# Kernel optimization log

Measured on AMD Instinct MI355X. Metric: run time of the kernel, lower is better.

## Reference

```python
import jax, jax.numpy as jnp
import numpy as np

B = 1024      # batch
D_NUM = 100   # numeric features
N_CAT = 20    # categorical features
CARD = 100    # cardinality per categorical feature
D = 1024      # d_token
DH = 675      # int(d_token * 0.66)
NT = D_NUM + 1 + N_CAT  # 121 tokens (CLS + numeric + categorical)
E = 4         # num_experts
K = 2         # top_k
MID = 512     # ResidualHead mid dim = max(D//2, 16)
RH = 256      # router/alpha hidden = max(D//4, 16)


def _ln(x, g, b):
    m = x.mean(-1, keepdims=True)
    v = ((x - m) ** 2).mean(-1, keepdims=True)
    return (x - m) * jax.lax.rsqrt(v + 1e-5) * g + b


def setup_inputs() -> dict:
    key = jax.random.key(0)
    ks = jax.random.split(key, 20)

    def n(i, shape, s=0.02):
        return jax.random.normal(ks[i], shape, dtype=jnp.float32) * s

    return dict(
        x_num=jax.random.normal(ks[0], (B, D_NUM), dtype=jnp.float32),
        x_cat=jax.random.randint(ks[1], (B, N_CAT), 0, CARD),
        tok_w=n(2, (D_NUM + 1, D), 0.05),
        tok_b=n(3, (D_NUM + N_CAT, D), 0.05),
        cat_emb=n(4, (N_CAT * CARD, D), 0.05),
        ln_g=jnp.ones((D,), jnp.float32), ln_b=jnp.zeros((D,), jnp.float32),
        lin0_w=n(5, (D, 2 * DH)), lin0_b=jnp.zeros((2 * DH,), jnp.float32),
        sgu_ln_g=jnp.ones((DH,), jnp.float32), sgu_ln_b=jnp.zeros((DH,), jnp.float32),
        sgu_w=n(6, (NT, NT), 0.05), sgu_b=jnp.zeros((NT,), jnp.float32),
        lin1_w=n(7, (DH, D)), lin1_b=jnp.zeros((D,), jnp.float32),
        r_w1=n(8, (D, RH)), r_b1=jnp.zeros((RH,), jnp.float32),
        r_w2=n(9, (RH, E)), r_b2=jnp.zeros((E,), jnp.float32),
        a_w1=n(10, (D, RH)), a_b1=jnp.zeros((RH,), jnp.float32),
        a_w2=n(11, (RH, 1)), a_b2=jnp.full((1,), -4.0, jnp.float32),
        base_w=n(12, (D, 1)), base_b=jnp.zeros((1,), jnp.float32),
        gh_w1=n(13, (D, MID), 0.001), gh_b1=jnp.zeros((MID,), jnp.float32),
        gh_w2=n(14, (MID, 1), 0.001), gh_b2=jnp.zeros((1,), jnp.float32),
        ex_w1=n(15, (E, D, MID), 0.001), ex_b1=jnp.zeros((E, MID), jnp.float32),
        ex_w2=n(16, (E, MID), 0.001), ex_b2=jnp.zeros((E,), jnp.float32),
    )


def reference(x_num, x_cat, tok_w, tok_b, cat_emb, ln_g, ln_b, lin0_w, lin0_b,
              sgu_ln_g, sgu_ln_b, sgu_w, sgu_b, lin1_w, lin1_b,
              r_w1, r_b1, r_w2, r_b2, a_w1, a_b1, a_w2, a_b2,
              base_w, base_b, gh_w1, gh_b1, gh_w2, gh_b2,
              ex_w1, ex_b1, ex_w2, ex_b2):
    # ---- Tokenizer ----
    offsets = jnp.arange(N_CAT) * CARD
    xn = jnp.concatenate([jnp.ones((x_num.shape[0], 1), x_num.dtype), x_num], axis=1)  # [B, D_NUM+1]
    x = tok_w[None] * xn[:, :, None]                                  # [B, D_NUM+1, D]
    x = jnp.concatenate([x, cat_emb[x_cat + offsets[None]]], axis=1)  # [B, NT, D]
    bias_full = jnp.concatenate([jnp.zeros((1, D), tok_b.dtype), tok_b], axis=0)
    x = x + bias_full[None]
    # ---- gMLP layer (n_layers=1) ----
    xr = x
    h = _ln(x, ln_g, ln_b)
    h = jax.nn.gelu(h @ lin0_w + lin0_b, approximate=False)           # [B, NT, 2*DH]
    u, v = h[..., :DH], h[..., DH:]
    v = _ln(v, sgu_ln_g, sgu_ln_b)
    # SGU token-mixing: out[b,s,d] = sum_t v[b,t,d] * W[s,t] + bias[s]
    v = jnp.einsum('btd,st->bsd', v, sgu_w) + sgu_b[None, :, None]
    x = (u * v) @ lin1_w + lin1_b
    x = x + xr
    # ---- pooled hidden (CLS token) ----
    hidden = jax.nn.gelu(_ln(x[:, 0], ln_g, ln_b), approximate=False)  # [B, D]
    # ---- router + top-k sparsification ----
    logits = jax.nn.relu(hidden @ r_w1 + r_b1) @ r_w2 + r_b2           # [B, E]
    dense = jax.nn.softmax(logits, axis=-1)
    vals, idx = jax.lax.top_k(dense, K)
    sparse = jnp.zeros_like(dense).at[jnp.arange(dense.shape[0])[:, None], idx].set(vals)
    rw = sparse / jnp.clip(sparse.sum(-1, keepdims=True), 1e-8)
    # ---- local experts (small residual heads, vectorized over E) ----
    eh = jax.nn.relu(jnp.einsum('bd,edm->bem', hidden, ex_w1) + ex_b1[None])
    eo = jnp.einsum('bem,em->be', eh, ex_w2) + ex_b2[None]             # [B, E]
    local = (rw * eo).sum(-1, keepdims=True)                           # [B, 1]
    # ---- global residual, alpha gate, base head ----
    glob = jax.nn.relu(hidden @ gh_w1 + gh_b1) @ gh_w2 + gh_b2
    alpha = jax.nn.sigmoid(jax.nn.relu(hidden @ a_w1 + a_b1) @ a_w2 + a_b2)
    y_base = hidden @ base_w + base_b
    return y_base + alpha * (glob + local)                             # [B, 1]
```

## Files before the change

### kernel.cpp

```cpp
#include <hip/hip_runtime.h>
#include <math.h>

#define B_SZ 1024

typedef __attribute__((ext_vector_type(8))) short bf16x8;
typedef __attribute__((ext_vector_type(4))) float f32x4;
typedef __attribute__((ext_vector_type(4))) float floatx4;
typedef __attribute__((ext_vector_type(4))) unsigned short ushortx4;

#define GLOAD16(src, dst) __builtin_amdgcn_global_load_lds( \
    (const __attribute__((address_space(1))) void*)(src), \
    (__attribute__((address_space(3))) void*)(dst), 16, 0, 0)

__device__ __forceinline__ unsigned short f2bf(float f) {
  unsigned int u = __float_as_uint(f);
  u += 0x7fff + ((u >> 16) & 1);
  return (unsigned short)(u >> 16);
}
__device__ __forceinline__ float bf2f(unsigned short b) {
  return __uint_as_float(((unsigned int)b) << 16);
}
__device__ __forceinline__ float gelu_exact(float x) {
  return 0.5f * x * (1.0f + erff(x * 0.70710678118654752f));
}
__device__ __forceinline__ float gelu_fast(float x) {
  const float c0 = 2.3022586f;
  const float c1 = 0.10295465f;
  float z = x * __builtin_fmaf(x * x, c1, c0);
  float e = __builtin_amdgcn_exp2f(z);
  float r = __builtin_amdgcn_rcpf(e + 1.0f);
  return __builtin_fmaf(-x, r, x);
}
__device__ __forceinline__ float wred(float v) {
#pragma unroll
  for (int o = 32; o > 0; o >>= 1) v += __shfl_xor(v, o, 64);
  return v;
}

struct PrepArgs {
  const float* src[10];
  unsigned short* dst[10];
  int ldin[10]; int coff[10]; int Nsrc[10]; int Ksrc[10]; int Kp[10];
  int nbx[10]; int blk0[11];
};

__global__ __launch_bounds__(256)
void prep_all(PrepArgs J,
              const float* __restrict__ tok_w, const float* __restrict__ tok_b,
              const float* __restrict__ cat_emb,
              const float* __restrict__ ln_g, const float* __restrict__ ln_b,
              const float* __restrict__ r_b1, const float* __restrict__ a_b1,
              const float* __restrict__ gh_b1, const float* __restrict__ ex_b1,
              unsigned short* __restrict__ Amat,
              float* __restrict__ nstat, float* __restrict__ cstat,
              float* __restrict__ bcat)
{
  const int bid = blockIdx.x;
  const int tid = threadIdx.x;
  const int lane = tid & 63;
  const int NT = J.blk0[10];
  if (bid < NT) {
    __shared__ float tile[64][65];
    int j = 0;
    while (bid >= J.blk0[j + 1]) ++j;
    const int bx = bid - J.blk0[j];
    const int k0 = (bx % J.nbx[j]) * 64;
    const int n0 = (bx / J.nbx[j]) * 64;
    const float* in = J.src[j];
    unsigned short* out = J.dst[j];
    const int ldin = J.ldin[j], coff = J.coff[j], Nsrc = J.Nsrc[j], Ksrc = J.Ksrc[j], Kp = J.Kp[j];
    const int kx = tid & 63;
    const int ry = tid >> 6;
    for (int r = ry; r < 64; r += 4) {
      const int k = k0 + r;
      const int n = n0 + kx;
      tile[r][kx] = (k < Ksrc && n < Nsrc) ? in[(size_t)k * ldin + coff + n] : 0.f;
    }
    __syncthreads();
    for (int r = ry; r < 64; r += 4) {
      const int n = n0 + r;
      const int k = k0 + kx;
      out[(size_t)n * Kp + k] = f2bf(tile[kx][r]);
    }
  } else if (bid < NT + 576) {
    const int r = (bid - NT) * 4 + (tid >> 6);
    if (r >= 2304) return;
    unsigned short* out = Amat + (size_t)r * 1024;
    for (int k = lane * 4; k < 1024; k += 256) {
      floatx4 g = *(const floatx4*)(ln_g + k);
      floatx4 v;
      if (r <= 100) {
        floatx4 a = *(const floatx4*)(tok_w + (size_t)r * 1024 + k);
#pragma unroll
        for (int q = 0; q < 4; q++) v[q] = a[q] * g[q];
      } else if (r <= 200) {
        floatx4 a = *(const floatx4*)(tok_b + (size_t)(r - 101) * 1024 + k);
#pragma unroll
        for (int q = 0; q < 4; q++) v[q] = a[q] * g[q];
      } else if (r <= 2200) {
        const int j = r - 201;
        const int c = j / 100;
        floatx4 a = *(const floatx4*)(cat_emb + (size_t)j * 1024 + k);
        floatx4 bq = *(const floatx4*)(tok_b + (size_t)(100 + c) * 1024 + k);
#pragma unroll
        for (int q = 0; q < 4; q++) v[q] = (a[q] + bq[q]) * g[q];
      } else if (r == 2201) {
        v = g;
      } else if (r == 2202) {
        v = *(const floatx4*)(ln_b + k);
      } else {
        v[0] = 0.f; v[1] = 0.f; v[2] = 0.f; v[3] = 0.f;
      }
      ushortx4 o;
#pragma unroll
      for (int q = 0; q < 4; q++) o[q] = f2bf(v[q]);
      *(ushortx4*)(out + k) = o;
    }
  } else if (bid < NT + 576 + 526) {
    const int w = (bid - NT - 576) * 4 + (tid >> 6);
    if (w >= 2101) return;
    if (w <= 100) {
      const int t = w;
      const float* wr = tok_w + (size_t)t * 1024;
      const float* br = (t >= 1) ? (tok_b + (size_t)(t - 1) * 1024) : nullptr;
      float sw = 0, sww = 0, sb = 0, sbb = 0, swb = 0;
      for (int k = lane * 4; k < 1024; k += 256) {
        floatx4 a = *(const floatx4*)(wr + k);
#pragma unroll
        for (int q = 0; q < 4; q++) { sw += a[q]; sww += a[q] * a[q]; }
        if (br) {
          floatx4 bq = *(const floatx4*)(br + k);
#pragma unroll
          for (int q = 0; q < 4; q++) { sb += bq[q]; sbb += bq[q] * bq[q]; swb += a[q] * bq[q]; }
        }
      }
      sw = wred(sw); sww = wred(sww); sb = wred(sb); sbb = wred(sbb); swb = wred(swb);
      if (lane == 0) {
        float* ns = nstat + (size_t)t * 5;
        ns[0] = sw; ns[1] = sww; ns[2] = sb; ns[3] = sbb; ns[4] = swb;
      }
    } else {
      const int j = w - 101;
      const int c = j / 100;
      const float* ar = cat_emb + (size_t)j * 1024;
      const float* br = tok_b + (size_t)(100 + c) * 1024;
      float s1 = 0, s2 = 0;
      for (int k = lane * 4; k < 1024; k += 256) {
        floatx4 a = *(const floatx4*)(ar + k);
        floatx4 bq = *(const floatx4*)(br + k);
#pragma unroll
        for (int q = 0; q < 4; q++) { const float v = a[q] + bq[q]; s1 += v; s2 += v * v; }
      }
      s1 = wred(s1); s2 = wred(s2);
      if (lane == 0) { cstat[(size_t)j * 2] = s1; cstat[(size_t)j * 2 + 1] = s2; }
    }
  } else {
    const int n = (bid - NT - 1102) * 256 + tid;
    if (n >= 3072) return;
    float v;
    if (n < 256) v = r_b1[n];
    else if (n < 512) v = a_b1[n - 256];
    else if (n < 1024) v = gh_b1[n - 512];
    else v = ex_b1[n - 1024];
    bcat[n] = v;
  }
}

template<int EPI>
__device__ __forceinline__
void gemm_body(int bid, const unsigned short* __restrict__ A, long pitchA,
               const unsigned short* __restrict__ Bw, int K,
               const float* __restrict__ bias, int bias_off,
               const float* __restrict__ extra,
               int NB, int Nvalid, int ldo,
               float* __restrict__ outf, unsigned short* __restrict__ outb)
{
  __shared__ unsigned short As[128 * 32];
  __shared__ unsigned short Bs[128 * 32];
  const int tid = threadIdx.x, lane = tid & 63, wv = tid >> 6;
  const int nb = bid % NB, mb = bid / NB;
  const int m0 = mb * 128, n0 = nb * 128;
  const int wr = (wv >> 1) << 6, wc = (wv & 1) << 6;
  const int fr = lane & 15, fq = lane >> 4;
  const int c0 = wv * 2;
  const int srow = lane >> 2;
  const int sk = (lane & 3) << 3;

  const unsigned short* a0 = A + (size_t)(m0 + c0 * 16 + srow) * pitchA + sk;
  const unsigned short* a1 = A + (size_t)(m0 + (c0 + 1) * 16 + srow) * pitchA + sk;
  const unsigned short* b0p = Bw + (size_t)(n0 + c0 * 16 + srow) * K + sk;
  const unsigned short* b1p = Bw + (size_t)(n0 + (c0 + 1) * 16 + srow) * K + sk;

  f32x4 acc[4][4] = {};
  for (int k0 = 0; k0 < K; k0 += 32) {
    __syncthreads();
    GLOAD16(a0 + k0, &As[c0 * 512]);
    GLOAD16(a1 + k0, &As[(c0 + 1) * 512]);
    GLOAD16(b0p + k0, &Bs[c0 * 512]);
    GLOAD16(b1p + k0, &Bs[(c0 + 1) * 512]);
    __syncthreads();
    bf16x8 af[4], bw_[4];
#pragma unroll
    for (int i = 0; i < 4; i++) {
      af[i]  = *(const bf16x8*)&As[(wr + i * 16 + fr) * 32 + fq * 8];
      bw_[i] = *(const bf16x8*)&Bs[(wc + i * 16 + fr) * 32 + fq * 8];
    }
#pragma unroll
    for (int i = 0; i < 4; i++)
#pragma unroll
      for (int j = 0; j < 4; j++)
        acc[i][j] = __builtin_amdgcn_mfma_f32_16x16x32_bf16(af[i], bw_[j], acc[i][j], 0, 0, 0);
  }

#pragma unroll
  for (int i = 0; i < 4; i++)
#pragma unroll
    for (int j = 0; j < 4; j++) {
      const int n = n0 + wc + j * 16 + fr;
      if (n >= ldo) continue;
      const bool valid = (n < Nvalid);
      const float bv = (EPI == 3) ? 0.f : (valid ? bias[bias_off + n] : 0.f);
      const float ev = (EPI == 0) ? extra[n] : 0.f;
#pragma unroll
      for (int q = 0; q < 4; q++) {
        const int m = m0 + wr + i * 16 + fq * 4 + q;
        const float a = acc[i][j][q];
        if (EPI == 0) {
          outf[(size_t)m * ldo + n] = a + bv + ev;
        } else if (EPI == 1) {
          outb[(size_t)m * ldo + n] = f2bf(fmaxf(a + bv, 0.f));
        } else {
          outf[(size_t)m * ldo + n] = a;
        }
      }
    }
}

template<int EPI>
__global__ __launch_bounds__(256)
void gemm_gl(const unsigned short* __restrict__ A, long pitchA,
             const unsigned short* __restrict__ Bw, int K,
             const float* __restrict__ bias, int bias_off,
             const float* __restrict__ extra,
             int NB, int Nvalid, int ldo,
             float* __restrict__ outf, unsigned short* __restrict__ outb)
{
  gemm_body<EPI>(blockIdx.x, A, pitchA, Bw, K, bias, bias_off, extra, NB, Nvalid, ldo, outf, outb);
}

__device__ __forceinline__
void u_const_body(int bid, const unsigned short* __restrict__ w0u, const float* __restrict__ nstat,
                  const float* __restrict__ tok_w, const float* __restrict__ ln_g,
                  const float* __restrict__ ln_b, const float* __restrict__ lin0_b,
                  float* __restrict__ ucon)
{
  __shared__ float xk[1024];
  const int tid = threadIdx.x, lane = tid & 63, wv = tid >> 6;
  const float m = nstat[0] * (1.f / 1024.f);
  const float ex2 = nstat[1] * (1.f / 1024.f);
  const float rs = rsqrtf(ex2 - m * m + 1e-5f);
  for (int k = tid; k < 1024; k += 256)
    xk[k] = bf2f(f2bf((tok_w[k] - m) * rs * ln_g[k] + ln_b[k]));
  __syncthreads();
  const int c = bid * 4 + wv;
  if (c >= 704) return;
  if (c >= 675) { if (lane == 0) ucon[c] = 0.f; return; }
  const unsigned short* wr = w0u + (size_t)c * 1024;
  float s = 0.f;
  for (int k = lane; k < 1024; k += 64) s += bf2f(wr[k]) * xk[k];
  s = wred(s);
  if (lane == 0) ucon[c] = gelu_exact(s + lin0_b[c]);
}

__global__ __launch_bounds__(256)
void tab_and_u(const unsigned short* __restrict__ Amat, const unsigned short* __restrict__ w0v,
               float* __restrict__ TAB,
               const unsigned short* __restrict__ w0u, const float* __restrict__ nstat,
               const float* __restrict__ tok_w, const float* __restrict__ ln_g,
               const float* __restrict__ ln_b, const float* __restrict__ lin0_b,
               float* __restrict__ ucon)
{
  if (blockIdx.x < 108)
    gemm_body<3>(blockIdx.x, Amat, 1024, w0v, 1024, nullptr, 0, nullptr, 6, 768, 768, TAB, nullptr);
  else
    u_const_body(blockIdx.x - 108, w0u, nstat, tok_w, ln_g, ln_b, lin0_b, ucon);
}

__global__ __launch_bounds__(256)
void cat_rows(const float* __restrict__ TAB, const float* __restrict__ nstat,
              const float* __restrict__ cstat, const float* __restrict__ lin0_b,
              const float* __restrict__ sgu_w,
              float* __restrict__ catval, float* __restrict__ catsc,
              float* __restrict__ wss_g)
{
  const int r = blockIdx.x * 4 + (threadIdx.x >> 6);
  const int lane = threadIdx.x & 63;
  if (r == 2001) {
    float s = (lane < 121) ? sgu_w[lane] : 0.f;
    if (lane + 64 < 121) s += sgu_w[lane + 64];
    s = wred(s);
    if (lane == 0) wss_g[0] = s;
    return;
  }
  if (r > 2001) return;
  float m, ex2;
  const float* T1;
  if (r < 2000) {
    m = cstat[(size_t)r * 2] * (1.f / 1024.f);
    ex2 = cstat[(size_t)r * 2 + 1] * (1.f / 1024.f);
    T1 = TAB + (size_t)(201 + r) * 768;
  } else {
    m = nstat[0] * (1.f / 1024.f);
    ex2 = nstat[1] * (1.f / 1024.f);
    T1 = TAB;
  }
  const float rs = rsqrtf(ex2 - m * m + 1e-5f);
  const float ga = -m * rs;
  const float* R = TAB + (size_t)2201 * 768;
  const float* C = TAB + (size_t)2202 * 768;
  const int dl = lane << 2;
  float s = 0.f, ss = 0.f;
  float* outp = catval + (size_t)r * 768;
#pragma unroll
  for (int ch = 0; ch < 3; ch++) {
    const int d = ch * 256 + dl;
    floatx4 t1 = *(const floatx4*)(T1 + d);
    floatx4 rr = *(const floatx4*)(R + d);
    floatx4 cc = *(const floatx4*)(C + d);
    floatx4 o;
#pragma unroll
    for (int q = 0; q < 4; q++) {
      const int dd = d + q;
      const float c2 = (dd < 675) ? (cc[q] + lin0_b[675 + dd]) : 0.f;
      const float pre = __builtin_fmaf(rs, t1[q], __builtin_fmaf(ga, rr[q], c2));
      const float g = (dd < 675) ? gelu_fast(pre) : 0.f;
      o[q] = g; s += g; ss = __builtin_fmaf(g, g, ss);
    }
    *(floatx4*)(outp + d) = o;
  }
  s = wred(s); ss = wred(ss);
  const float mu = s * (1.f / 675.f);
  const float rho = rsqrtf(ss * (1.f / 675.f) - mu * mu + 1e-5f);
  if (lane == 0) { catsc[(size_t)r * 2] = mu; catsc[(size_t)r * 2 + 1] = rho; }
}

__global__ __launch_bounds__(512, 4)
void fused_v4(const float* __restrict__ TAB, const float* __restrict__ nstat,
              const float* __restrict__ catsc, const float* __restrict__ catval,
              const float* __restrict__ x_num, const int* __restrict__ x_cat,
              const float* __restrict__ sgu_ln_g, const float* __restrict__ sgu_ln_b,
              const float* __restrict__ sgu_w, const float* __restrict__ sgu_b,
              const float* __restrict__ lin0_b, const float* __restrict__ ucon,
              const float* __restrict__ wss_g,
              unsigned short* __restrict__ uv)
{
  const int b = blockIdx.x;
  const int tid = threadIdx.x, lane = tid & 63, wv = tid >> 6;
  __shared__ float Rls[768], Cls[768];
  __shared__ float alf[100], bet[100], gam[100], swt[100];
  __shared__ float wrc[21], catkb[21];
  __shared__ int catrowS[21];
  __shared__ float accw[8][768];
  __shared__ float kbw[8];

  for (int d = tid; d < 768; d += 512) {
    Rls[d] = (d < 675) ? TAB[(size_t)2201 * 768 + d] : 0.f;
    Cls[d] = (d < 675) ? (TAB[(size_t)2202 * 768 + d] + lin0_b[675 + d]) : 0.f;
  }
  if (tid < 100) {
    const int tt = tid;
    const float sc = x_num[b * 100 + tt];
    const float* ns = nstat + (size_t)(tt + 1) * 5;
    const float m = (sc * ns[0] + ns[2]) * (1.f / 1024.f);
    const float ex2 = (sc * sc * ns[1] + 2.f * sc * ns[4] + ns[3]) * (1.f / 1024.f);
    const float rs = rsqrtf(ex2 - m * m + 1e-5f);
    alf[tt] = rs * sc; bet[tt] = rs; gam[tt] = -m * rs;
    swt[tt] = sgu_w[tt + 1];
  } else if (tid < 121) {
    const int ii = tid - 100;
    int row; float sw;
    if (ii < 20) { row = x_cat[b * 20 + ii] + 100 * ii; sw = sgu_w[101 + ii]; }
    else { row = 2000; sw = sgu_w[0]; }
    const float mu = catsc[(size_t)row * 2], rho = catsc[(size_t)row * 2 + 1];
    const float wr = sw * rho;
    wrc[ii] = wr; catkb[ii] = wr * mu; catrowS[ii] = row;
  }
  __syncthreads();

  float acc[12] = {};
  float kb = 0.f;
  const int dl = lane << 2;

  for (int i = 0; i < 7; i++) {
    const int tA = wv + 16 * i;
    if (tA >= 100) break;
    const int tB = tA + 8;
    const bool hB = (tB < 100);
    const int tBs = hB ? tB : tA;
    const float aA = alf[tA], eA = bet[tA], gA = gam[tA];
    const float aB = alf[tBs], eB = bet[tBs], gB = gam[tBs];
    const float* T1A = TAB + (size_t)(tA + 1) * 768;
    const float* T2A = TAB + (size_t)(101 + tA) * 768;
    const float* T1B = TAB + (size_t)(tBs + 1) * 768;
    const float* T2B = TAB + (size_t)(101 + tBs) * 768;
    float vA[12], vB[12];
    float sA = 0.f, qA = 0.f, sB = 0.f, qB = 0.f;
#pragma unroll
    for (int ch = 0; ch < 3; ch++) {
      const int d = ch * 256 + dl;
      floatx4 t1a = *(const floatx4*)(T1A + d);
      floatx4 t2a = *(const floatx4*)(T2A + d);
      floatx4 t1b = *(const floatx4*)(T1B + d);
      floatx4 t2b = *(const floatx4*)(T2B + d);
      floatx4 rr = *(const floatx4*)(&Rls[d]);
      floatx4 cc = *(const floatx4*)(&Cls[d]);
#pragma unroll
      for (int q = 0; q < 4; q++) {
        const float g0 = gelu_fast(__builtin_fmaf(aA, t1a[q], __builtin_fmaf(eA, t2a[q], __builtin_fmaf(gA, rr[q], cc[q]))));
        vA[ch * 4 + q] = g0; sA += g0; qA = __builtin_fmaf(g0, g0, qA);
        const float g1 = gelu_fast(__builtin_fmaf(aB, t1b[q], __builtin_fmaf(eB, t2b[q], __builtin_fmaf(gB, rr[q], cc[q]))));
        vB[ch * 4 + q] = g1; sB += g1; qB = __builtin_fmaf(g1, g1, qB);
      }
    }
    sA = wred(sA); qA = wred(qA); sB = wred(sB); qB = wred(qB);
    const float swA = swt[tA];
    const float swB = hB ? swt[tBs] : 0.f;
    const float muA = sA * (1.f / 675.f);
    const float wA = swA * rsqrtf(qA * (1.f / 675.f) - muA * muA + 1e-5f);
    const float muB = sB * (1.f / 675.f);
    const float wB = swB * rsqrtf(qB * (1.f / 675.f) - muB * muB + 1e-5f);
#pragma unroll
    for (int q = 0; q < 12; q++)
      acc[q] = __builtin_fmaf(wA, vA[q], __builtin_fmaf(wB, vB[q], acc[q]));
    kb = __builtin_fmaf(wA, muA, __builtin_fmaf(wB, muB, kb));
  }

  for (int i = 0; i < 3; i++) {
    const int ii = wv + 8 * i;
    if (ii >= 21) break;
    const float wr = wrc[ii];
    const float* cv = catval + (size_t)catrowS[ii] * 768;
#pragma unroll
    for (int ch = 0; ch < 3; ch++) {
      floatx4 v = *(const floatx4*)(cv + ch * 256 + dl);
#pragma unroll
      for (int q = 0; q < 4; q++) acc[ch * 4 + q] = __builtin_fmaf(wr, v[q], acc[ch * 4 + q]);
    }
  }
  if (lane == 0) kbw[wv] = kb;

#pragma unroll
  for (int ch = 0; ch < 3; ch++)
    *(floatx4*)&accw[wv][ch * 256 + dl] = *(const floatx4*)&acc[ch * 4];
  __syncthreads();

  float kbs = 0.f;
#pragma unroll
  for (int w = 0; w < 8; w++) kbs += kbw[w];
#pragma unroll
  for (int i = 0; i < 21; i++) kbs += catkb[i];
  const float sb0 = sgu_b[0];
  const float wss = wss_g[0];
  for (int d = tid; d < 704; d += 512) {
    unsigned short o = 0;
    if (d < 675) {
      float a = 0.f;
#pragma unroll
      for (int w = 0; w < 8; w++) a += accw[w][d];
      const float v0 = sgu_ln_g[d] * (a - kbs) + sgu_ln_b[d] * wss + sb0;
      o = f2bf(ucon[d] * v0);
    }
    uv[(size_t)b * 704 + d] = o;
  }
}

__global__ __launch_bounds__(256)
void ln_gelu_hidden(const float* __restrict__ xfin,
                    const float* __restrict__ ln_g, const float* __restrict__ ln_b,
                    const float* __restrict__ base_w,
                    unsigned short* __restrict__ hid_bf, float* __restrict__ base_y)
{
  const int w = (blockIdx.x * 256 + threadIdx.x) >> 6;
  const int lane = threadIdx.x & 63;
  if (w >= B_SZ) return;
  const float* row = xfin + (size_t)w * 1024;
  float s = 0.f, ss = 0.f;
  for (int k = lane; k < 1024; k += 64) { float v = row[k]; s += v; ss += v * v; }
  s = wred(s); ss = wred(ss);
  const float m = s * (1.f / 1024.f);
  const float var = ss * (1.f / 1024.f) - m * m;
  const float rs = rsqrtf(var + 1e-5f);
  float bacc = 0.f;
  for (int k = lane; k < 1024; k += 64) {
    float v = gelu_fast((row[k] - m) * rs * ln_g[k] + ln_b[k]);
    hid_bf[(size_t)w * 1024 + k] = f2bf(v);
    bacc = __builtin_fmaf(v, base_w[k], bacc);
  }
  bacc = wred(bacc);
  if (lane == 0) base_y[w] = bacc;
}

__global__ __launch_bounds__(256)
void final_head(const unsigned short* __restrict__ H1, const float* __restrict__ base_y,
                const float* __restrict__ r_w2, const float* __restrict__ r_b2,
                const float* __restrict__ a_w2, const float* __restrict__ a_b2,
                const float* __restrict__ gh_w2, const float* __restrict__ gh_b2,
                const float* __restrict__ ex_w2, const float* __restrict__ ex_b2,
                const float* __restrict__ base_b,
                float* __restrict__ out)
{
  const int b = blockIdx.x;
  const int tid = threadIdx.x;
  const unsigned short* h1 = H1 + (size_t)b * 3072;
  float p[10];
#pragma unroll
  for (int i = 0; i < 10; i++) p[i] = 0.f;
  {
    const int m = tid;
    const float hr = bf2f(h1[m]);
    p[0] = hr * r_w2[m * 4 + 0];
    p[1] = hr * r_w2[m * 4 + 1];
    p[2] = hr * r_w2[m * 4 + 2];
    p[3] = hr * r_w2[m * 4 + 3];
    const float ha = bf2f(h1[256 + m]);
    p[4] = ha * a_w2[m];
  }
  for (int m = tid; m < 512; m += 256) {
    p[5] += bf2f(h1[512 + m]) * gh_w2[m];
#pragma unroll
    for (int e = 0; e < 4; e++)
      p[6 + e] += bf2f(h1[1024 + e * 512 + m]) * ex_w2[e * 512 + m];
  }

  __shared__ float red[10][4];
  const int lane = tid & 63, wv = tid >> 6;
#pragma unroll
  for (int i = 0; i < 10; i++) {
    const float v = wred(p[i]);
    if (lane == 0) red[i][wv] = v;
  }
  __syncthreads();
  if (tid == 0) {
    float s[10];
#pragma unroll
    for (int i = 0; i < 10; i++) s[i] = red[i][0] + red[i][1] + red[i][2] + red[i][3];
    float lg[4];
#pragma unroll
    for (int e = 0; e < 4; e++) lg[e] = s[e] + r_b2[e];
    const float mx = fmaxf(fmaxf(lg[0], lg[1]), fmaxf(lg[2], lg[3]));
    float den[4]; float dsum = 0.f;
#pragma unroll
    for (int e = 0; e < 4; e++) { den[e] = expf(lg[e] - mx); dsum += den[e]; }
#pragma unroll
    for (int e = 0; e < 4; e++) den[e] /= dsum;
    int i1 = 0;
    for (int e = 1; e < 4; e++) if (den[e] > den[i1]) i1 = e;
    int i2 = -1;
    for (int e = 0; e < 4; e++) { if (e == i1) continue; if (i2 < 0 || den[e] > den[i2]) i2 = e; }
    float eo[4];
#pragma unroll
    for (int e = 0; e < 4; e++) eo[e] = s[6 + e] + ex_b2[e];
    const float v1 = den[i1], v2 = den[i2];
    const float ssum = fmaxf(v1 + v2, 1e-8f);
    const float local = (v1 * eo[i1] + v2 * eo[i2]) / ssum;
    const float glob = s[5] + gh_b2[0];
    const float alpha = 1.0f / (1.0f + expf(-(s[4] + a_b2[0])));
    out[b] = base_y[b] + base_b[0] + alpha * (glob + local);
  }
}

extern "C" void kernel_launch(void* const* d_in, const int* in_sizes, int n_in,
                              void* d_out, int out_size, void* d_ws, size_t ws_size,
                              hipStream_t stream)
{
  const float* x_num  = (const float*)d_in[0];
  const int*   x_cat  = (const int*)d_in[1];
  const float* tok_w  = (const float*)d_in[2];
  const float* tok_b  = (const float*)d_in[3];
  const float* cat_emb= (const float*)d_in[4];
  const float* ln_g   = (const float*)d_in[5];
  const float* ln_b   = (const float*)d_in[6];
  const float* lin0_w = (const float*)d_in[7];
  const float* lin0_b = (const float*)d_in[8];
  const float* sgu_ln_g = (const float*)d_in[9];
  const float* sgu_ln_b = (const float*)d_in[10];
  const float* sgu_w  = (const float*)d_in[11];
  const float* sgu_b  = (const float*)d_in[12];
  const float* lin1_w = (const float*)d_in[13];
  const float* lin1_b = (const float*)d_in[14];
  const float* r_w1   = (const float*)d_in[15];
  const float* r_b1   = (const float*)d_in[16];
  const float* r_w2   = (const float*)d_in[17];
  const float* r_b2   = (const float*)d_in[18];
  const float* a_w1   = (const float*)d_in[19];
  const float* a_b1   = (const float*)d_in[20];
  const float* a_w2   = (const float*)d_in[21];
  const float* a_b2   = (const float*)d_in[22];
  const float* base_w = (const float*)d_in[23];
  const float* base_b = (const float*)d_in[24];
  const float* gh_w1  = (const float*)d_in[25];
  const float* gh_b1  = (const float*)d_in[26];
  const float* gh_w2  = (const float*)d_in[27];
  const float* gh_b2  = (const float*)d_in[28];
  const float* ex_w1  = (const float*)d_in[29];
  const float* ex_b1  = (const float*)d_in[30];
  const float* ex_w2  = (const float*)d_in[31];
  const float* ex_b2  = (const float*)d_in[32];
  (void)in_sizes; (void)n_in; (void)out_size; (void)ws_size;

  char* ws = (char*)d_ws;
  size_t off = 0;
  auto alloc = [&](size_t bytes) { void* p = ws + off; off += (bytes + 255) & ~(size_t)255; return p; };

  unsigned short* w0v  = (unsigned short*)alloc((size_t)768 * 1024 * 2);
  unsigned short* w0u  = (unsigned short*)alloc((size_t)768 * 1024 * 2);
  unsigned short* w1t  = (unsigned short*)alloc((size_t)1024 * 704 * 2);
  unsigned short* wcat = (unsigned short*)alloc((size_t)3072 * 1024 * 2);
  float* bcat          = (float*)alloc((size_t)3072 * 4);
  unsigned short* Amat = (unsigned short*)alloc((size_t)2304 * 1024 * 2);
  float* TAB           = (float*)alloc((size_t)2304 * 768 * 4);
  float* nstat         = (float*)alloc((size_t)101 * 5 * 4);
  float* cstat         = (float*)alloc((size_t)2000 * 2 * 4);
  float* catval        = (float*)alloc((size_t)2001 * 768 * 4);
  float* catsc         = (float*)alloc((size_t)2001 * 2 * 4);
  float* ucon          = (float*)alloc((size_t)704 * 4);
  float* wss_g         = (float*)alloc((size_t)4);
  unsigned short* uv   = (unsigned short*)alloc((size_t)B_SZ * 704 * 2);
  float* xfin          = (float*)alloc((size_t)B_SZ * 1024 * 4);
  float* base_y        = (float*)alloc((size_t)B_SZ * 4);
  unsigned short* hidb = (unsigned short*)alloc((size_t)B_SZ * 1024 * 2);
  unsigned short* H1   = (unsigned short*)alloc((size_t)B_SZ * 3072 * 2);

  const dim3 blk(256);

  PrepArgs J;
  auto setJ = [&](int i, const float* s, unsigned short* d, int ldin, int coff,
                  int Nsrc, int Ksrc, int Kp, int nbx, int nby) {
    J.src[i] = s; J.dst[i] = d; J.ldin[i] = ldin; J.coff[i] = coff;
    J.Nsrc[i] = Nsrc; J.Ksrc[i] = Ksrc; J.Kp[i] = Kp; J.nbx[i] = nbx;
    J.blk0[i + 1] = J.blk0[i] + nbx * nby;
  };
  J.blk0[0] = 0;
  setJ(0, lin0_w, w0v, 1350, 675, 675, 1024, 1024, 16, 12);
  setJ(1, lin0_w, w0u, 1350, 0,   675, 1024, 1024, 16, 12);
  setJ(2, lin1_w, w1t, 1024, 0,  1024,  675,  704, 11, 16);
  setJ(3, r_w1,  wcat,                          256, 0, 256, 1024, 1024, 16, 4);
  setJ(4, a_w1,  wcat + (size_t)256 * 1024,     256, 0, 256, 1024, 1024, 16, 4);
  setJ(5, gh_w1, wcat + (size_t)512 * 1024,     512, 0, 512, 1024, 1024, 16, 8);
  for (int e = 0; e < 4; e++)
    setJ(6 + e, ex_w1 + (size_t)e * 1024 * 512,
         wcat + (size_t)(1024 + e * 512) * 1024, 512, 0, 512, 1024, 1024, 16, 8);

  const int nprep = J.blk0[10] + 576 + 526 + 12;
  prep_all<<<nprep, blk, 0, stream>>>(J, tok_w, tok_b, cat_emb, ln_g, ln_b,
      r_b1, a_b1, gh_b1, ex_b1, Amat, nstat, cstat, bcat);

  tab_and_u<<<284, blk, 0, stream>>>(Amat, w0v, TAB, w0u, nstat, tok_w, ln_g, ln_b, lin0_b, ucon);

  cat_rows<<<501, blk, 0, stream>>>(TAB, nstat, cstat, lin0_b, sgu_w, catval, catsc, wss_g);

  fused_v4<<<B_SZ, dim3(512), 0, stream>>>(TAB, nstat, catsc, catval, x_num, x_cat,
      sgu_ln_g, sgu_ln_b, sgu_w, sgu_b, lin0_b, ucon, wss_g, uv);

  gemm_gl<0><<<8 * 8, blk, 0, stream>>>(uv, 704, w1t, 704,
      lin1_b, 0, tok_w, 8, 1024, 1024, xfin, nullptr);
  ln_gelu_hidden<<<B_SZ / 4, blk, 0, stream>>>(xfin, ln_g, ln_b, base_w, hidb, base_y);
  gemm_gl<1><<<8 * 24, blk, 0, stream>>>(hidb, 1024, wcat, 1024,
      bcat, 0, nullptr, 24, 3072, 3072, nullptr, H1);

  final_head<<<B_SZ, blk, 0, stream>>>(H1, base_y, r_w2, r_b2, a_w2, a_b2, gh_w2, gh_b2,
                                       ex_w2, ex_b2, base_b, (float*)d_out);
}
```

Baseline: 157.5 us.

## Shrink GEMM tiles to 64x64 and halve fused token-mixing block size

After: 165.6 us. +5.1%, slower.

```diff
diff --git a/kernel.cpp b/kernel.cpp
--- a/kernel.cpp
+++ b/kernel.cpp
@@ -168,58 +168,50 @@
 
 template<int EPI>
 __device__ __forceinline__
-void gemm_body(int bid, const unsigned short* __restrict__ A, long pitchA,
-               const unsigned short* __restrict__ Bw, int K,
-               const float* __restrict__ bias, int bias_off,
-               const float* __restrict__ extra,
-               int NB, int Nvalid, int ldo,
-               float* __restrict__ outf, unsigned short* __restrict__ outb)
-{
-  __shared__ unsigned short As[128 * 32];
-  __shared__ unsigned short Bs[128 * 32];
+void gemm64_body(int bid, const unsigned short* __restrict__ A, long pitchA,
+                 const unsigned short* __restrict__ Bw, int K,
+                 const float* __restrict__ bias, const float* __restrict__ extra,
+                 int NB, int Nvalid, int ldo,
+                 float* __restrict__ outf, unsigned short* __restrict__ outb)
+{
+  __shared__ unsigned short As[64 * 32];
+  __shared__ unsigned short Bs[64 * 32];
   const int tid = threadIdx.x, lane = tid & 63, wv = tid >> 6;
   const int nb = bid % NB, mb = bid / NB;
-  const int m0 = mb * 128, n0 = nb * 128;
-  const int wr = (wv >> 1) << 6, wc = (wv & 1) << 6;
+  const int m0 = mb * 64, n0 = nb * 64;
+  const int wr = (wv >> 1) << 5, wc = (wv & 1) << 5;
   const int fr = lane & 15, fq = lane >> 4;
-  const int c0 = wv * 2;
-  const int srow = lane >> 2;
-  const int sk = (lane & 3) << 3;
-
-  const unsigned short* a0 = A + (size_t)(m0 + c0 * 16 + srow) * pitchA + sk;
-  const unsigned short* a1 = A + (size_t)(m0 + (c0 + 1) * 16 + srow) * pitchA + sk;
-  const unsigned short* b0p = Bw + (size_t)(n0 + c0 * 16 + srow) * K + sk;
-  const unsigned short* b1p = Bw + (size_t)(n0 + (c0 + 1) * 16 + srow) * K + sk;
-
-  f32x4 acc[4][4] = {};
+
+  const unsigned short* srcA = A + (size_t)(m0 + (tid >> 2)) * pitchA + ((tid & 3) << 3);
+  const unsigned short* srcB = Bw + (size_t)(n0 + (tid >> 2)) * K + ((tid & 3) << 3);
+
+  f32x4 acc[2][2] = {};
   for (int k0 = 0; k0 < K; k0 += 32) {
     __syncthreads();
-    GLOAD16(a0 + k0, &As[c0 * 512]);
-    GLOAD16(a1 + k0, &As[(c0 + 1) * 512]);
-    GLOAD16(b0p + k0, &Bs[c0 * 512]);
-    GLOAD16(b1p + k0, &Bs[(c0 + 1) * 512]);
+    GLOAD16(srcA + k0, &As[tid * 8]);
+    GLOAD16(srcB + k0, &Bs[tid * 8]);
     __syncthreads();
-    bf16x8 af[4], bw_[4];
-#pragma unroll
-    for (int i = 0; i < 4; i++) {
+    bf16x8 af[2], bw_[2];
+#pragma unroll
+    for (int i = 0; i < 2; i++) {
       af[i]  = *(const bf16x8*)&As[(wr + i * 16 + fr) * 32 + fq * 8];
       bw_[i] = *(const bf16x8*)&Bs[(wc + i * 16 + fr) * 32 + fq * 8];
     }
 #pragma unroll
-    for (int i = 0; i < 4; i++)
-#pragma unroll
-      for (int j = 0; j < 4; j++)
+    for (int i = 0; i < 2; i++)
+#pragma unroll
+      for (int j = 0; j < 2; j++)
         acc[i][j] = __builtin_amdgcn_mfma_f32_16x16x32_bf16(af[i], bw_[j], acc[i][j], 0, 0, 0);
   }
 
 #pragma unroll
-  for (int i = 0; i < 4; i++)
-#pragma unroll
-    for (int j = 0; j < 4; j++) {
+  for (int i = 0; i < 2; i++)
+#pragma unroll
+    for (int j = 0; j < 2; j++) {
       const int n = n0 + wc + j * 16 + fr;
       if (n >= ldo) continue;
       const bool valid = (n < Nvalid);
-      const float bv = (EPI == 3) ? 0.f : (valid ? bias[bias_off + n] : 0.f);
+      const float bv = (EPI == 3) ? 0.f : (valid ? bias[n] : 0.f);
       const float ev = (EPI == 0) ? extra[n] : 0.f;
 #pragma unroll
       for (int q = 0; q < 4; q++) {
@@ -238,14 +230,13 @@
 
 template<int EPI>
 __global__ __launch_bounds__(256)
-void gemm_gl(const unsigned short* __restrict__ A, long pitchA,
-             const unsigned short* __restrict__ Bw, int K,
-             const float* __restrict__ bias, int bias_off,
-             const float* __restrict__ extra,
-             int NB, int Nvalid, int ldo,
-             float* __restrict__ outf, unsigned short* __restrict__ outb)
-{
-  gemm_body<EPI>(blockIdx.x, A, pitchA, Bw, K, bias, bias_off, extra, NB, Nvalid, ldo, outf, outb);
+void gemm64(const unsigned short* __restrict__ A, long pitchA,
+            const unsigned short* __restrict__ Bw, int K,
+            const float* __restrict__ bias, const float* __restrict__ extra,
+            int NB, int Nvalid, int ldo,
+            float* __restrict__ outf, unsigned short* __restrict__ outb)
+{
+  gemm64_body<EPI>(blockIdx.x, A, pitchA, Bw, K, bias, extra, NB, Nvalid, ldo, outf, outb);
 }
 
 __device__ __forceinline__
@@ -280,10 +271,10 @@
                const float* __restrict__ ln_b, const float* __restrict__ lin0_b,
                float* __restrict__ ucon)
 {
-  if (blockIdx.x < 108)
-    gemm_body<3>(blockIdx.x, Amat, 1024, w0v, 1024, nullptr, 0, nullptr, 6, 768, 768, TAB, nullptr);
+  if (blockIdx.x < 432)
+    gemm64_body<3>(blockIdx.x, Amat, 1024, w0v, 1024, nullptr, nullptr, 12, 768, 768, TAB, nullptr);
   else
-    u_const_body(blockIdx.x - 108, w0u, nstat, tok_w, ln_g, ln_b, lin0_b, ucon);
+    u_const_body(blockIdx.x - 432, w0u, nstat, tok_w, ln_g, ln_b, lin0_b, ucon);
 }
 
 __global__ __launch_bounds__(256)
@@ -344,8 +335,8 @@
   if (lane == 0) { catsc[(size_t)r * 2] = mu; catsc[(size_t)r * 2 + 1] = rho; }
 }
 
-__global__ __launch_bounds__(512, 4)
-void fused_v4(const float* __restrict__ TAB, const float* __restrict__ nstat,
+__global__ __launch_bounds__(256, 8)
+void fused_v5(const float* __restrict__ TAB, const float* __restrict__ nstat,
               const float* __restrict__ catsc, const float* __restrict__ catval,
               const float* __restrict__ x_num, const int* __restrict__ x_cat,
               const float* __restrict__ sgu_ln_g, const float* __restrict__ sgu_ln_b,
@@ -360,10 +351,10 @@
   __shared__ float alf[100], bet[100], gam[100], swt[100];
   __shared__ float wrc[21], catkb[21];
   __shared__ int catrowS[21];
-  __shared__ float accw[8][768];
-  __shared__ float kbw[8];
-
-  for (int d = tid; d < 768; d += 512) {
+  __shared__ float accw[4][768];
+  __shared__ float kbw[4];
+
+  for (int d = tid; d < 768; d += 256) {
     Rls[d] = (d < 675) ? TAB[(size_t)2201 * 768 + d] : 0.f;
     Cls[d] = (d < 675) ? (TAB[(size_t)2202 * 768 + d] + lin0_b[675 + d]) : 0.f;
   }
@@ -391,10 +382,10 @@
   float kb = 0.f;
   const int dl = lane << 2;
 
-  for (int i = 0; i < 7; i++) {
-    const int tA = wv + 16 * i;
+  for (int i = 0; i < 13; i++) {
+    const int tA = wv + 8 * i;
     if (tA >= 100) break;
-    const int tB = tA + 8;
+    const int tB = tA + 4;
     const bool hB = (tB < 100);
     const int tBs = hB ? tB : tA;
     const float aA = alf[tA], eA = bet[tA], gA = gam[tA];
@@ -435,8 +426,8 @@
     kb = __builtin_fmaf(wA, muA, __builtin_fmaf(wB, muB, kb));
   }
 
-  for (int i = 0; i < 3; i++) {
-    const int ii = wv + 8 * i;
+  for (int i = 0; i < 6; i++) {
+    const int ii = wv + 4 * i;
     if (ii >= 21) break;
     const float wr = wrc[ii];
     const float* cv = catval + (size_t)catrowS[ii] * 768;
@@ -454,19 +445,15 @@
     *(floatx4*)&accw[wv][ch * 256 + dl] = *(const floatx4*)&acc[ch * 4];
   __syncthreads();
 
-  float kbs = 0.f;
-#pragma unroll
-  for (int w = 0; w < 8; w++) kbs += kbw[w];
+  float kbs = kbw[0] + kbw[1] + kbw[2] + kbw[3];
 #pragma unroll
   for (int i = 0; i < 21; i++) kbs += catkb[i];
   const float sb0 = sgu_b[0];
   const float wss = wss_g[0];
-  for (int d = tid; d < 704; d += 512) {
+  for (int d = tid; d < 704; d += 256) {
     unsigned short o = 0;
     if (d < 675) {
-      float a = 0.f;
-#pragma unroll
-      for (int w = 0; w < 8; w++) a += accw[w][d];
+      const float a = accw[0][d] + accw[1][d] + accw[2][d] + accw[3][d];
       const float v0 = sgu_ln_g[d] * (a - kbs) + sgu_ln_b[d] * wss + sb0;
       o = f2bf(ucon[d] * v0);
     }
@@ -655,18 +642,18 @@
   prep_all<<<nprep, blk, 0, stream>>>(J, tok_w, tok_b, cat_emb, ln_g, ln_b,
       r_b1, a_b1, gh_b1, ex_b1, Amat, nstat, cstat, bcat);
 
-  tab_and_u<<<284, blk, 0, stream>>>(Amat, w0v, TAB, w0u, nstat, tok_w, ln_g, ln_b, lin0_b, ucon);
+  tab_and_u<<<608, blk, 0, stream>>>(Amat, w0v, TAB, w0u, nstat, tok_w, ln_g, ln_b, lin0_b, ucon);
 
   cat_rows<<<501, blk, 0, stream>>>(TAB, nstat, cstat, lin0_b, sgu_w, catval, catsc, wss_g);
 
-  fused_v4<<<B_SZ, dim3(512), 0, stream>>>(TAB, nstat, catsc, catval, x_num, x_cat,
+  fused_v5<<<B_SZ, blk, 0, stream>>>(TAB, nstat, catsc, catval, x_num, x_cat,
       sgu_ln_g, sgu_ln_b, sgu_w, sgu_b, lin0_b, ucon, wss_g, uv);
 
-  gemm_gl<0><<<8 * 8, blk, 0, stream>>>(uv, 704, w1t, 704,
-      lin1_b, 0, tok_w, 8, 1024, 1024, xfin, nullptr);
+  gemm64<0><<<16 * 16, blk, 0, stream>>>(uv, 704, w1t, 704,
+      lin1_b, tok_w, 16, 1024, 1024, xfin, nullptr);
   ln_gelu_hidden<<<B_SZ / 4, blk, 0, stream>>>(xfin, ln_g, ln_b, base_w, hidb, base_y);
-  gemm_gl<1><<<8 * 24, blk, 0, stream>>>(hidb, 1024, wcat, 1024,
-      bcat, 0, nullptr, 24, 3072, 3072, nullptr, H1);
+  gemm64<1><<<16 * 48, blk, 0, stream>>>(hidb, 1024, wcat, 1024,
+      bcat, nullptr, 48, 3072, 3072, nullptr, H1);
 
   final_head<<<B_SZ, blk, 0, stream>>>(H1, base_y, r_w2, r_b2, a_w2, a_b2, gh_w2, gh_b2,
                                        ex_w2, ex_b2, base_b, (float*)d_out);
```
